# Kernel tuning notes

Hardware: AMD Instinct MI355X
Metric: run time of the kernel (lower is better)

## Reference

```python
import jax, jax.numpy as jnp
import numpy as np

ODE_UNFOLDS = 6   # ncps LTCCell default
EPS = 1e-8
BATCH = 4096

def _conv(x, w, b, stride, pad):
    y = jax.lax.conv_general_dilated(x, w, (stride, stride), [(pad, pad), (pad, pad)],
                                     dimension_numbers=('NCHW', 'OIHW', 'NCHW'))
    return y + b[None, :, None, None]

def _bn(x, g, bta, m, v):
    # eval-mode batchnorm (running stats)
    inv = g * jax.lax.rsqrt(v + 1e-5)
    return x * inv[None, :, None, None] + (bta - m * inv)[None, :, None, None]

def _maxpool2(x):
    return jax.lax.reduce_window(x, -jnp.inf, jax.lax.max, (1, 1, 2, 2), (1, 1, 2, 2), 'VALID')

def _forward(x, conv1_w, conv1_b, conv2_w, conv2_b, bn2_g, bn2_b, bn2_m, bn2_v,
             conv3_w, conv3_b, conv4_w, conv4_b, bn4_g, bn4_b, bn4_m, bn4_v,
             input_w, input_b, sensory_mu, sensory_sigma, sensory_w, sensory_erev, sensory_mask,
             mu, sigma, w, erev, mask, gleak, vleak, cm, output_w, output_b):
    h = jax.nn.relu(_conv(x, conv1_w, conv1_b, 1, 0))                                            # [B,16,26,26]
    h = jax.nn.relu(_bn(_conv(h, conv2_w, conv2_b, 2, 2), bn2_g, bn2_b, bn2_m, bn2_v))           # [B,32,14,14]
    h = jax.nn.relu(_conv(h, conv3_w, conv3_b, 2, 2))                                            # [B,64,7,7]
    h = _maxpool2(jax.nn.relu(_bn(_conv(h, conv4_w, conv4_b, 2, 2), bn4_g, bn4_b, bn4_m, bn4_v)))  # [B,128,2,2]
    seq = h.reshape(-1, 32, 16)                                                                  # [B,T=32,F=16]
    # --- LTC cell (ncps fused ODE solver) ---
    xin = seq * input_w + input_b                                                                # affine input mapping
    # sensory synapses depend only on the input -> precompute for all timesteps
    sact = jax.nn.softplus(sensory_w) * jax.nn.sigmoid((xin[..., None] - sensory_mu) * sensory_sigma) * sensory_mask  # [B,T,16,19]
    wnum_s = jnp.einsum('btsn,sn->btn', sact, sensory_erev)   # [B,T,19]
    wden_s = jnp.sum(sact, axis=2)                            # [B,T,19]
    w_pos = jax.nn.softplus(w) * mask                         # [pre=19,post=19]
    gl = jax.nn.softplus(gleak)
    cm_t = jax.nn.softplus(cm) * ODE_UNFOLDS                  # cm / (elapsed_time=1.0 / unfolds)
    def tstep(v, nd):
        wns, wds = nd
        def unfold(v2, _):
            wa = w_pos * jax.nn.sigmoid((v2[..., None] - mu) * sigma)   # [B,19,19]
            num = cm_t * v2 + gl * vleak + jnp.sum(wa * erev, axis=1) + wns
            den = cm_t + gl + jnp.sum(wa, axis=1) + wds
            return num / (den + EPS), None
        v, _ = jax.lax.scan(unfold, v, None, length=ODE_UNFOLDS)
        return v, None
    h0 = jnp.zeros((seq.shape[0], 19), seq.dtype)
    vT, _ = jax.lax.scan(tstep, h0, (jnp.swapaxes(wnum_s, 0, 1), jnp.swapaxes(wden_s, 0, 1)))
    # out[:, -1, :] == output mapping of final state; motor neurons are the first 2
    return vT[:, :2] * output_w + output_b


def setup_inputs() -> dict:
    key = jax.random.key(0)
    ks = jax.random.split(key, 16)
    rng = np.random.default_rng(0)
    u = lambda k, s, lo, hi: jax.random.uniform(k, s, jnp.float32, lo, hi)
    n = lambda k, s, sc: jax.random.normal(k, s, jnp.float32) * sc
    inp = {}
    inp['x'] = jax.random.normal(ks[0], (BATCH, 1, 28, 28), jnp.float32)
    inp['conv1_w'] = n(ks[1], (16, 1, 3, 3), 0.3); inp['conv1_b'] = jnp.zeros(16)
    inp['conv2_w'] = n(ks[2], (32, 16, 3, 3), 0.08); inp['conv2_b'] = jnp.zeros(32)
    inp['bn2_g'] = jnp.ones(32); inp['bn2_b'] = jnp.zeros(32)
    inp['bn2_m'] = jnp.zeros(32); inp['bn2_v'] = jnp.ones(32)
    inp['conv3_w'] = n(ks[3], (64, 32, 5, 5), 0.035); inp['conv3_b'] = jnp.zeros(64)
    inp['conv4_w'] = n(ks[4], (128, 64, 5, 5), 0.025); inp['conv4_b'] = jnp.zeros(128)
    inp['bn4_g'] = jnp.ones(128); inp['bn4_b'] = jnp.zeros(128)
    inp['bn4_m'] = jnp.zeros(128); inp['bn4_v'] = jnp.ones(128)
    inp['input_w'] = jnp.ones(16); inp['input_b'] = jnp.zeros(16)
    # ncps LTCCell init ranges
    inp['sensory_mu'] = u(ks[5], (16, 19), 0.3, 0.8)
    inp['sensory_sigma'] = u(ks[6], (16, 19), 3.0, 8.0)
    inp['sensory_w'] = u(ks[7], (16, 19), 0.001, 1.0)
    inp['sensory_erev'] = jnp.asarray(rng.choice([-1.0, 1.0], (16, 19)).astype(np.float32))
    inp['sensory_mask'] = jnp.asarray((rng.random((16, 19)) < 0.35).astype(np.float32))
    inp['mu'] = u(ks[8], (19, 19), 0.3, 0.8)
    inp['sigma'] = u(ks[9], (19, 19), 3.0, 8.0)
    inp['w'] = u(ks[10], (19, 19), 0.001, 1.0)
    inp['erev'] = jnp.asarray(rng.choice([-1.0, 1.0], (19, 19)).astype(np.float32))
    inp['mask'] = jnp.asarray((rng.random((19, 19)) < 0.35).astype(np.float32))
    inp['gleak'] = u(ks[11], (19,), 0.001, 1.0)
    inp['vleak'] = u(ks[12], (19,), -0.2, 0.2)
    inp['cm'] = u(ks[13], (19,), 0.4, 0.6)
    inp['output_w'] = jnp.ones(2); inp['output_b'] = jnp.zeros(2)
    return inp


def reference(x, conv1_w, conv1_b, conv2_w, conv2_b, bn2_g, bn2_b, bn2_m, bn2_v,
              conv3_w, conv3_b, conv4_w, conv4_b, bn4_g, bn4_b, bn4_m, bn4_v,
              input_w, input_b, sensory_mu, sensory_sigma, sensory_w, sensory_erev, sensory_mask,
              mu, sigma, w, erev, mask, gleak, vleak, cm, output_w, output_b):
    return _forward(x, conv1_w, conv1_b, conv2_w, conv2_b, bn2_g, bn2_b, bn2_m, bn2_v,
                    conv3_w, conv3_b, conv4_w, conv4_b, bn4_g, bn4_b, bn4_m, bn4_v,
                    input_w, input_b, sensory_mu, sensory_sigma, sensory_w, sensory_erev, sensory_mask,
                    mu, sigma, w, erev, mask, gleak, vleak, cm, output_w, output_b)
```

## Files before the change

kernel.cpp:

```cpp
#include <hip/hip_runtime.h>

#define BATCH 4096
typedef unsigned short u16_t;

#define P_SWM   0
#define P_SWME  304
#define P_WP    608
#define P_WPE   969
#define P_GL    1330
#define P_GLVL  1349
#define P_CMT   1368
#define P_SC2   1392
#define P_SH2   1424
#define P_SC4   1456
#define P_SH4   1584

#define OFF_PAR 0L
#define OFF_B2F 2048L
#define OFF_B3F 6656L
#define OFF_B4F 57856L
#define OFF_DYN 262656L

typedef __attribute__((ext_vector_type(8))) short short8;
typedef __attribute__((ext_vector_type(16))) float f32x16;
typedef __attribute__((ext_vector_type(4))) float f32x4;
#define MFMA(a, b, c) __builtin_amdgcn_mfma_f32_32x32x16_bf16(a, b, c, 0, 0, 0)
#define MFMA16(a, b, c) __builtin_amdgcn_mfma_f32_16x16x32_bf16(a, b, c, 0, 0, 0)

#define PERM_HI(w1, w0) __builtin_amdgcn_perm((w1), (w0), 0x05040100u)
#define PERM_LO(w1, w0) __builtin_amdgcn_perm((w1), (w0), 0x07060302u)

union U8 { unsigned u[4]; short8 v; };
union A4 { f32x4 v; float f[4]; };

__device__ __forceinline__ float sigmoidf_(float x) {
    return 1.0f / (1.0f + __expf(-x));
}
__device__ __forceinline__ float softplusf_(float x) { return log1pf(__expf(x)); }

__device__ __forceinline__ unsigned rne16(unsigned u) {
    return (u + 0x7FFFu + ((u >> 16) & 1u)) & 0xFFFF0000u;
}
__device__ __forceinline__ unsigned splitpack(float f) {
    unsigned uh = rne16(__float_as_uint(f));
    float rsd = f - __uint_as_float(uh);
    unsigned ur = rne16(__float_as_uint(rsd));
    return (uh >> 16) | ur;
}
__device__ __forceinline__ u16_t bfhalf(float v, int pl) {
    unsigned uh = rne16(__float_as_uint(v));
    if (pl == 0) return (u16_t)(uh >> 16);
    float rsd = v - __uint_as_float(uh);
    return (u16_t)(rne16(__float_as_uint(rsd)) >> 16);
}

__global__ __launch_bounds__(256) void k_prep(
    const float* __restrict__ w2, const float* __restrict__ w3, const float* __restrict__ w4,
    const float* __restrict__ sw, const float* __restrict__ serev, const float* __restrict__ smask,
    const float* __restrict__ w,  const float* __restrict__ erev,  const float* __restrict__ mask,
    const float* __restrict__ gleak, const float* __restrict__ vleak, const float* __restrict__ cm,
    const float* __restrict__ b2, const float* __restrict__ g2, const float* __restrict__ be2,
    const float* __restrict__ m2, const float* __restrict__ v2,
    const float* __restrict__ b4, const float* __restrict__ g4, const float* __restrict__ be4,
    const float* __restrict__ m4, const float* __restrict__ v4,
    float* __restrict__ ws) {
    int gid = blockIdx.x * 256 + threadIdx.x, stride = gridDim.x * 256;
    u16_t* b2f = (u16_t*)(ws + OFF_B2F);
    u16_t* b3f = (u16_t*)(ws + OFF_B3F);
    u16_t* b4f = (u16_t*)(ws + OFF_B4F);
    for (int i = gid; i < 9216; i += stride) {
        int j = i & 7, ln = (i >> 3) & 63;
        int r = i >> 9;
        int s = r % 9, pl = r / 9;
        int k = s * 16 + (ln >> 5) * 8 + j;
        int tap = k >> 4, ci = k & 15;
        int co = ln & 31;
        b2f[i] = bfhalf(w2[(co * 16 + ci) * 9 + tap], pl);
    }
    for (int i = gid; i < 102400; i += stride) {
        int j = i & 7, ln = (i >> 3) & 63;
        int t = i >> 9;
        int tap = t % 25, r = t / 25;
        int nt = r & 3, pl = r >> 2;
        int co = nt * 16 + (ln & 15);
        int ci = (ln >> 4) * 8 + j;
        b3f[i] = bfhalf(w3[(co * 32 + ci) * 25 + tap], pl);
    }
    for (int i = gid; i < 409600; i += stride) {
        int j = i & 7, ln = (i >> 3) & 63;
        int t = i >> 9;
        int ks = t % 50, r = t / 50;
        int nt = r & 7, pl = r >> 3;
        int co = nt * 16 + (ln & 15);
        int tap = ks >> 1;
        int ci = (ks & 1) * 32 + (ln >> 4) * 8 + j;
        b4f[i] = bfhalf(w4[(co * 64 + ci) * 25 + tap], pl);
    }
    if (blockIdx.x == 0) {
        float* par = ws + OFF_PAR;
        int tid = threadIdx.x;
        for (int i = tid; i < 304; i += 256) {
            float v_ = softplusf_(sw[i]) * smask[i];
            par[P_SWM + i] = v_;
            par[P_SWME + i] = v_ * serev[i];
        }
        for (int i = tid; i < 361; i += 256) {
            float v_ = softplusf_(w[i]) * mask[i];
            par[P_WP + i] = v_;
            par[P_WPE + i] = v_ * erev[i];
        }
        for (int i = tid; i < 19; i += 256) {
            float g = softplusf_(gleak[i]);
            par[P_GL + i] = g;
            par[P_GLVL + i] = g * vleak[i];
            par[P_CMT + i] = softplusf_(cm[i]) * 6.0f;
        }
        for (int i = tid; i < 32; i += 256) {
            float inv = g2[i] * __frsqrt_rn(v2[i] + 1e-5f);
            par[P_SC2 + i] = inv;
            par[P_SH2 + i] = (b2[i] - m2[i]) * inv + be2[i];
        }
        for (int i = tid; i < 128; i += 256) {
            float inv = g4[i] * __frsqrt_rn(v4[i] + 1e-5f);
            par[P_SC4 + i] = inv;
            par[P_SH4 + i] = (b4[i] - m4[i]) * inv + be4[i];
        }
    }
}

__global__ __launch_bounds__(512, 6) void k_conv12(
    const float* __restrict__ x, const float* __restrict__ w1, const float* __restrict__ b1,
    const float* __restrict__ ws, unsigned* __restrict__ h2g) {
    __shared__ float xs[784];
    __shared__ unsigned h1s[11509];
    const float* par = ws + OFF_PAR;
    int b = blockIdx.x, tid = threadIdx.x;
    {
        for (int i = tid; i < 784; i += 512) xs[i] = x[(long)b * 784 + i];
        if (tid < 17) h1s[676 * 17 + tid] = 0u;
    }
    __syncthreads();
    {
        int co = tid >> 5, slot = tid & 31;
        float wr[9];
        #pragma unroll
        for (int i = 0; i < 9; i++) wr[i] = w1[co * 9 + i];
        float bb = b1[co];
        for (int k = 0; k < 22; k++) {
            int px = slot + (k << 5);
            if (px >= 676) break;
            int oh = px / 26, ow = px % 26;
            float s = bb;
            #pragma unroll
            for (int kh = 0; kh < 3; kh++)
                #pragma unroll
                for (int kw = 0; kw < 3; kw++)
                    s = fmaf(xs[(oh + kh) * 28 + ow + kw], wr[kh * 3 + kw], s);
            h1s[px * 17 + co] = splitpack(fmaxf(s, 0.f));
        }
    }
    __syncthreads();
    {
        int wv = tid >> 6, lane = tid & 63;
        int mloc = lane & 31, hf = lane >> 5, half8 = hf * 8;
        const u16_t* B2 = (const u16_t*)(ws + OFF_B2F);
        const short8* pb = (const short8*)B2 + lane;
        float sc = par[P_SC2 + mloc], sh = par[P_SH2 + mloc];
        int mt = wv;
        if (mt < 7) {
            int px = mt * 32 + mloc;
            bool pxok = px < 196;
            int pxc = pxok ? px : 195;
            int oh = pxc / 14, ow = pxc % 14;
            int ihb = oh * 2 - 2, iwb = ow * 2 - 2;
            f32x16 acc;
            #pragma unroll
            for (int i = 0; i < 16; i++) acc[i] = 0.f;
            #pragma unroll
            for (int s = 0; s < 9; s++) {
                int kh = s / 3, kw = s % 3;
                int ih = ihb + kh, iw = iwb + kw;
                bool ok = pxok && ((unsigned)ih < 26u) && ((unsigned)iw < 26u);
                int abase = (ok ? (ih * 26 + iw) * 17 : 676 * 17) + half8;
                unsigned w_[8];
                #pragma unroll
                for (int j = 0; j < 8; j++) w_[j] = h1s[abase + j];
                U8 ah, al;
                #pragma unroll
                for (int d = 0; d < 4; d++) {
                    ah.u[d] = PERM_HI(w_[2 * d + 1], w_[2 * d]);
                    al.u[d] = PERM_LO(w_[2 * d + 1], w_[2 * d]);
                }
                short8 bh = pb[s * 64];
                short8 bl = pb[(9 + s) * 64];
                acc = MFMA(ah.v, bh, acc);
                acc = MFMA(ah.v, bl, acc);
                acc = MFMA(al.v, bh, acc);
                acc = MFMA(al.v, bl, acc);
            }
            #pragma unroll
            for (int r5 = 0; r5 < 16; r5++) {
                int row = (r5 & 3) + 8 * (r5 >> 2) + 4 * hf;
                int pxw = mt * 32 + row;
                if (pxw < 196) {
                    float y = fmaxf(fmaf(acc[r5], sc, sh), 0.f);
                    h2g[(long)b * 6272 + pxw * 32 + mloc] = splitpack(y);
                }
            }
        }
    }
}

__global__ __launch_bounds__(256, 2) void k_conv34s(
    const unsigned* __restrict__ h2g, const float* __restrict__ b3g,
    const float* __restrict__ inw, const float* __restrict__ inb,
    const float* __restrict__ smu, const float* __restrict__ ssig,
    const float* __restrict__ ws,
    float* __restrict__ wn, float* __restrict__ wd, int nimg) {
    __shared__ unsigned h2s[12969];
    __shared__ unsigned h3s[6435];
    const float* par = ws + OFF_PAR;
    int b = blockIdx.x, tid = threadIdx.x;
    int g0 = b * 2;
    int g1 = (g0 + 1 < nimg) ? g0 + 1 : g0;
    {
        const unsigned* s0 = h2g + (long)g0 * 6272;
        const unsigned* s1 = h2g + (long)g1 * 6272;
        for (int i = tid; i < 12544; i += 256) {
            int img = i >= 6272;
            int r = img ? i - 6272 : i;
            h2s[img * 6468 + (r >> 5) * 33 + (r & 31)] = (img ? s1 : s0)[r];
        }
        if (tid < 33) h2s[12936 + tid] = 0u;
        if (tid < 65) h3s[6370 + tid] = 0u;
    }
    __syncthreads();
    int wv = tid >> 6, lane = tid & 63;
    int n16 = lane & 15, quad = lane >> 4, quad8 = quad * 8;

    {
        int img = wv & 1, mhalf = wv >> 1;
        int imgo = img * 6468;
        int mt0 = mhalf * 2;
        A4 acc[2][4];
        #pragma unroll
        for (int nt = 0; nt < 4; nt++) {
            float bi = b3g[nt * 16 + n16];
            #pragma unroll
            for (int r = 0; r < 4; r++) { acc[0][nt].f[r] = bi; acc[1][nt].f[r] = bi; }
        }
        int oh2[2], ow2[2];
        bool pxok[2];
        #pragma unroll
        for (int mi = 0; mi < 2; mi++) {
            int px = (mt0 + mi) * 16 + n16;
            pxok[mi] = px < 49;
            int pxc = pxok[mi] ? px : 48;
            oh2[mi] = (pxc / 7) * 2 - 2;
            ow2[mi] = (pxc % 7) * 2 - 2;
        }
        const short8* B3 = (const short8*)(const u16_t*)(ws + OFF_B3F);
        const short8* ph0 = B3 + (0 * 25) * 64 + lane;
        const short8* ph1 = B3 + (1 * 25) * 64 + lane;
        const short8* ph2 = B3 + (2 * 25) * 64 + lane;
        const short8* ph3 = B3 + (3 * 25) * 64 + lane;
        const short8* pl0 = B3 + (4 * 25) * 64 + lane;
        const short8* pl1 = B3 + (5 * 25) * 64 + lane;
        const short8* pl2 = B3 + (6 * 25) * 64 + lane;
        const short8* pl3 = B3 + (7 * 25) * 64 + lane;
        #pragma unroll
        for (int kh = 0; kh < 5; kh++) {
            #pragma unroll
            for (int kw = 0; kw < 5; kw++) {
                int s = (kh * 5 + kw) * 64;
                short8 bh0 = ph0[s], bh1 = ph1[s], bh2 = ph2[s], bh3 = ph3[s];
                short8 bl0 = pl0[s], bl1 = pl1[s], bl2 = pl2[s], bl3 = pl3[s];
                #pragma unroll
                for (int mi = 0; mi < 2; mi++) {
                    int ih = oh2[mi] + kh, iw = ow2[mi] + kw;
                    bool ok = pxok[mi] && ((unsigned)ih < 14u) && ((unsigned)iw < 14u);
                    int rowb = ok ? imgo + (ih * 14 + iw) * 33 : 12936;
                    const unsigned* ap = h2s + rowb + quad8;
                    unsigned w_[8];
                    #pragma unroll
                    for (int j = 0; j < 8; j++) w_[j] = ap[j];
                    U8 ah, al;
                    #pragma unroll
                    for (int d = 0; d < 4; d++) {
                        ah.u[d] = PERM_HI(w_[2 * d + 1], w_[2 * d]);
                        al.u[d] = PERM_LO(w_[2 * d + 1], w_[2 * d]);
                    }
                    acc[mi][0].v = MFMA16(ah.v, bh0, acc[mi][0].v);
                    acc[mi][0].v = MFMA16(ah.v, bl0, acc[mi][0].v);
                    acc[mi][0].v = MFMA16(al.v, bh0, acc[mi][0].v);
                    acc[mi][0].v = MFMA16(al.v, bl0, acc[mi][0].v);
                    acc[mi][1].v = MFMA16(ah.v, bh1, acc[mi][1].v);
                    acc[mi][1].v = MFMA16(ah.v, bl1, acc[mi][1].v);
                    acc[mi][1].v = MFMA16(al.v, bh1, acc[mi][1].v);
                    acc[mi][1].v = MFMA16(al.v, bl1, acc[mi][1].v);
                    acc[mi][2].v = MFMA16(ah.v, bh2, acc[mi][2].v);
                    acc[mi][2].v = MFMA16(ah.v, bl2, acc[mi][2].v);
                    acc[mi][2].v = MFMA16(al.v, bh2, acc[mi][2].v);
                    acc[mi][2].v = MFMA16(al.v, bl2, acc[mi][2].v);
                    acc[mi][3].v = MFMA16(ah.v, bh3, acc[mi][3].v);
                    acc[mi][3].v = MFMA16(ah.v, bl3, acc[mi][3].v);
                    acc[mi][3].v = MFMA16(al.v, bh3, acc[mi][3].v);
                    acc[mi][3].v = MFMA16(al.v, bl3, acc[mi][3].v);
                }
            }
        }
        #pragma unroll
        for (int mi = 0; mi < 2; mi++) {
            #pragma unroll
            for (int nt = 0; nt < 4; nt++) {
                int co = nt * 16 + n16;
                #pragma unroll
                for (int r = 0; r < 4; r++) {
                    int pxw = (mt0 + mi) * 16 + quad * 4 + r;
                    if (pxw < 49)
                        h3s[img * 3185 + pxw * 65 + co] = splitpack(fmaxf(acc[mi][nt].f[r], 0.f));
                }
            }
        }
    }
    __syncthreads();
    {
        int oh = n16 >> 2, ow = n16 & 3;
        int oh2 = oh * 2 - 2, ow2 = ow * 2 - 2;
        int nt0 = wv * 2, nt1 = nt0 + 1;
        A4 c[2][2];
        #pragma unroll
        for (int mi = 0; mi < 2; mi++)
            #pragma unroll
            for (int r = 0; r < 4; r++) { c[mi][0].f[r] = 0.f; c[mi][1].f[r] = 0.f; }
        const short8* B4 = (const short8*)(const u16_t*)(ws + OFF_B4F);
        const short8* ph0 = B4 + (nt0 * 50) * 64 + lane;
        const short8* ph1 = B4 + (nt1 * 50) * 64 + lane;
        const short8* pl0 = B4 + ((8 + nt0) * 50) * 64 + lane;
        const short8* pl1 = B4 + ((8 + nt1) * 50) * 64 + lane;
        #pragma unroll
        for (int kh = 0; kh < 5; kh++) {
            int ih = oh2 + kh;
            #pragma unroll
            for (int kw = 0; kw < 5; kw++) {
                int iw = ow2 + kw;
                bool ok = ((unsigned)ih < 7u) && ((unsigned)iw < 7u);
                #pragma unroll
                for (int ch = 0; ch < 2; ch++) {
                    int s = ((kh * 5 + kw) * 2 + ch) * 64;
                    short8 bh0 = ph0[s], bl0 = pl0[s];
                    short8 bh1 = ph1[s], bl1 = pl1[s];
                    #pragma unroll
                    for (int mi = 0; mi < 2; mi++) {
                        int rowb = ok ? mi * 3185 + (ih * 7 + iw) * 65 + ch * 32 : 6370;
                        const unsigned* ap = h3s + rowb + quad8;
                        unsigned w_[8];
                        #pragma unroll
                        for (int j = 0; j < 8; j++) w_[j] = ap[j];
                        U8 ah, al;
                        #pragma unroll
                        for (int d = 0; d < 4; d++) {
                            ah.u[d] = PERM_HI(w_[2 * d + 1], w_[2 * d]);
                            al.u[d] = PERM_LO(w_[2 * d + 1], w_[2 * d]);
                        }
                        c[mi][0].v = MFMA16(ah.v, bh0, c[mi][0].v);
                        c[mi][0].v = MFMA16(ah.v, bl0, c[mi][0].v);
                        c[mi][0].v = MFMA16(al.v, bh0, c[mi][0].v);
                        c[mi][0].v = MFMA16(al.v, bl0, c[mi][0].v);
                        c[mi][1].v = MFMA16(ah.v, bh1, c[mi][1].v);
                        c[mi][1].v = MFMA16(ah.v, bl1, c[mi][1].v);
                        c[mi][1].v = MFMA16(al.v, bh1, c[mi][1].v);
                        c[mi][1].v = MFMA16(al.v, bl1, c[mi][1].v);
                    }
                }
            }
        }
        __syncthreads();
        float* xin_s = (float*)h2s;
        #pragma unroll
        for (int mi = 0; mi < 2; mi++) {
            #pragma unroll
            for (int t2 = 0; t2 < 2; t2++) {
                int co = (t2 ? nt1 : nt0) * 16 + n16;
                float sc = par[P_SC4 + co], sh = par[P_SH4 + co];
                float y[4];
                #pragma unroll
                for (int r = 0; r < 4; r++) y[r] = fmaxf(fmaf(c[mi][t2].f[r], sc, sh), 0.f);
                float p0 = fmaxf(y[0], y[1]);
                float p1 = fmaxf(y[2], y[3]);
                p0 = fmaxf(p0, __shfl_xor(p0, 16));
                p1 = fmaxf(p1, __shfl_xor(p1, 16));
                if ((quad & 1) == 0) {
                    int ph_ = quad >> 1;
                    int ts = co >> 2;
                    int f0 = ((co & 3) << 2) + ph_ * 2;
                    xin_s[mi * 512 + ts * 16 + f0] = fmaf(p0, inw[f0], inb[f0]);
                    xin_s[mi * 512 + ts * 16 + f0 + 1] = fmaf(p1, inw[f0 + 1], inb[f0 + 1]);
                }
            }
        }
    }
    __syncthreads();
    const float* xin_s = (const float*)h2s;
    for (int idx = tid; idx < 1216; idx += 256) {
        int img = idx >= 608;
        int r = img ? idx - 608 : idx;
        int gi = g0 + img;
        if (gi >= nimg) break;
        int tt = r / 19, n = r - tt * 19;
        float nu = 0.f, de = 0.f;
        #pragma unroll
        for (int s = 0; s < 16; s++) {
            float sg = sigmoidf_((xin_s[img * 512 + tt * 16 + s] - smu[s * 19 + n]) * ssig[s * 19 + n]);
            nu = fmaf(par[P_SWME + s * 19 + n], sg, nu);
            de = fmaf(par[P_SWM + s * 19 + n], sg, de);
        }
        wn[((long)gi * 32 + tt) * 19 + n] = nu;
        wd[((long)gi * 32 + tt) * 19 + n] = de;
    }
}

__global__ __launch_bounds__(256, 2) void k_ltc(
    const float* __restrict__ mu_g, const float* __restrict__ sg_g,
    const float* __restrict__ ws,
    const float* __restrict__ wn, const float* __restrict__ wd,
    const float* __restrict__ outw, const float* __restrict__ outb,
    float* __restrict__ out, int img0, int nimg) {
    const float* par = ws + OFF_PAR;
    int tid = threadIdx.x, wave = tid >> 6, lane = tid & 63;
    int li = lane / 19, j = lane - li * 19;
    if (li > 2) { li = 2; j = 18; }
    int il = blockIdx.x * 12 + wave * 3 + li;
    int ilc = il < nimg ? il : nimg - 1;

    const float L2E = 1.44269504f;
    float aj[19], bj[19], wpj[19], wpej[19];
    #pragma unroll
    for (int i = 0; i < 19; i++) {
        float mu = mu_g[i * 19 + j];
        float sg = sg_g[i * 19 + j];
        aj[i] = -sg * L2E;
        bj[i] = mu * sg * L2E;
        wpj[i] = par[P_WP + i * 19 + j];
        wpej[i] = par[P_WPE + i * 19 + j];
    }
    float cmt = par[P_CMT + j], gl = par[P_GL + j], glvl = par[P_GLVL + j];
    float v = 0.f;
    long base0 = (long)ilc * 608 + j;
    float wns = wn[base0], wds = wd[base0];
    int lbase = li * 19;
    for (int t = 0; t < 32; t++) {
        float wns_n = 0.f, wds_n = 0.f;
        if (t < 31) {
            long basen = base0 + (t + 1) * 19;
            wns_n = wn[basen];
            wds_n = wd[basen];
        }
        #pragma unroll 1
        for (int u = 0; u < 6; u++) {
            float vi[19];
            #pragma unroll
            for (int i = 0; i < 19; i++) vi[i] = __shfl(v, lbase + i, 64);
            float sg[19];
            #pragma unroll
            for (int i = 0; i < 19; i++)
                sg[i] = __builtin_amdgcn_exp2f(fmaf(vi[i], aj[i], bj[i]));
            float n0 = 0.f, n1 = 0.f, d0 = 0.f, d1 = 0.f;
            #pragma unroll
            for (int i = 0; i < 19; i++) {
                float s = __builtin_amdgcn_rcpf(1.0f + sg[i]);
                if (i & 1) { n1 = fmaf(wpej[i], s, n1); d1 = fmaf(wpj[i], s, d1); }
                else       { n0 = fmaf(wpej[i], s, n0); d0 = fmaf(wpj[i], s, d0); }
            }
            float num = fmaf(cmt, v, glvl) + wns + (n0 + n1);
            float den = cmt + gl + wds + (d0 + d1);
            v = num * __builtin_amdgcn_rcpf(den + 1e-8f);
        }
        wns = wns_n; wds = wds_n;
    }
    if (j < 2 && il < nimg && lane < 57)
        out[(long)(img0 + il) * 2 + j] = fmaf(v, outw[j], outb[j]);
}

extern "C" void kernel_launch(void* const* d_in, const int* in_sizes, int n_in,
                              void* d_out, int out_size, void* d_ws, size_t ws_size,
                              hipStream_t stream) {
    const float* x    = (const float*)d_in[0];
    const float* w1   = (const float*)d_in[1];
    const float* b1   = (const float*)d_in[2];
    const float* w2   = (const float*)d_in[3];
    const float* b2   = (const float*)d_in[4];
    const float* g2   = (const float*)d_in[5];
    const float* be2  = (const float*)d_in[6];
    const float* m2   = (const float*)d_in[7];
    const float* v2   = (const float*)d_in[8];
    const float* w3   = (const float*)d_in[9];
    const float* b3   = (const float*)d_in[10];
    const float* w4   = (const float*)d_in[11];
    const float* b4   = (const float*)d_in[12];
    const float* g4   = (const float*)d_in[13];
    const float* be4  = (const float*)d_in[14];
    const float* m4   = (const float*)d_in[15];
    const float* v4   = (const float*)d_in[16];
    const float* inw  = (const float*)d_in[17];
    const float* inb  = (const float*)d_in[18];
    const float* smu  = (const float*)d_in[19];
    const float* ssig = (const float*)d_in[20];
    const float* sw   = (const float*)d_in[21];
    const float* serv = (const float*)d_in[22];
    const float* smk  = (const float*)d_in[23];
    const float* mu_  = (const float*)d_in[24];
    const float* sig_ = (const float*)d_in[25];
    const float* w_   = (const float*)d_in[26];
    const float* erev = (const float*)d_in[27];
    const float* mask = (const float*)d_in[28];
    const float* glk  = (const float*)d_in[29];
    const float* vlk  = (const float*)d_in[30];
    const float* cm   = (const float*)d_in[31];
    const float* outw = (const float*)d_in[32];
    const float* outb = (const float*)d_in[33];
    float* ws = (float*)d_ws;

    k_prep<<<64, 256, 0, stream>>>(w2, w3, w4, sw, serv, smk, w_, erev, mask,
                                   glk, vlk, cm, b2, g2, be2, m2, v2,
                                   b4, g4, be4, m4, v4, ws);

    long avail = (long)(ws_size / 4) - OFF_DYN;
    long per = 6272 + 1216;
    int chunk = (int)(avail / per);
    if (chunk > BATCH) chunk = BATCH;
    if (chunk < 2) chunk = 2;

    float* wnp = ws + OFF_DYN;
    float* wdp = wnp + (long)chunk * 608;
    unsigned* h2 = (unsigned*)(wdp + (long)chunk * 608);

    for (int c0 = 0; c0 < BATCH; c0 += chunk) {
        int n = (BATCH - c0 < chunk) ? (BATCH - c0) : chunk;
        k_conv12<<<n, 512, 0, stream>>>(x + (long)c0 * 784, w1, b1, ws, h2);
        k_conv34s<<<(n + 1) / 2, 256, 0, stream>>>(h2, b3, inw, inb, smu, ssig, ws,
                                                   wnp, wdp, n);
        k_ltc<<<(n + 11) / 12, 256, 0, stream>>>(mu_, sig_, ws, wnp, wdp, outw, outb,
                                                 (float*)d_out, c0, n);
    }
}
```

Before: 570.3 us.

## Switch LTC ODE path to fp64 and drop low-low split-bf16 MFMA terms

```diff
diff --git a/kernel.cpp b/kernel.cpp
--- a/kernel.cpp
+++ b/kernel.cpp
@@ -1,25 +1,26 @@
 #include <hip/hip_runtime.h>
+#include <math.h>
 
 #define BATCH 4096
 typedef unsigned short u16_t;
 
-#define P_SWM   0
-#define P_SWME  304
-#define P_WP    608
-#define P_WPE   969
-#define P_GL    1330
-#define P_GLVL  1349
-#define P_CMT   1368
 #define P_SC2   1392
 #define P_SH2   1424
 #define P_SC4   1456
 #define P_SH4   1584
+#define P_GL64   1712
+#define P_GLVL64 1750
+#define P_CMT64  1788
+#define P_WP64   1826
+#define P_WPE64  2548
+#define P_SWM64  3270
+#define P_SWME64 3878
 
 #define OFF_PAR 0L
-#define OFF_B2F 2048L
-#define OFF_B3F 6656L
-#define OFF_B4F 57856L
-#define OFF_DYN 262656L
+#define OFF_B2F 4608L
+#define OFF_B3F 9216L
+#define OFF_B4F 60416L
+#define OFF_DYN 265216L
 
 typedef __attribute__((ext_vector_type(8))) short short8;
 typedef __attribute__((ext_vector_type(16))) float f32x16;
@@ -33,11 +34,6 @@
 union U8 { unsigned u[4]; short8 v; };
 union A4 { f32x4 v; float f[4]; };
 
-__device__ __forceinline__ float sigmoidf_(float x) {
-    return 1.0f / (1.0f + __expf(-x));
-}
-__device__ __forceinline__ float softplusf_(float x) { return log1pf(__expf(x)); }
-
 __device__ __forceinline__ unsigned rne16(unsigned u) {
     return (u + 0x7FFFu + ((u >> 16) & 1u)) & 0xFFFF0000u;
 }
@@ -52,6 +48,20 @@
     if (pl == 0) return (u16_t)(uh >> 16);
     float rsd = v - __uint_as_float(uh);
     return (u16_t)(rne16(__float_as_uint(rsd)) >> 16);
+}
+__device__ __forceinline__ double softplus64(double x) { return log1p(exp(x)); }
+
+__device__ __forceinline__ double sigmoid64(double arg) {
+    double na = -arg;
+    float yf = (float)na * 1.44269504f;
+    float e32 = __builtin_amdgcn_exp2f(yf);
+    double ey = fma(na, 1.4426950408889634, -(double)yf);
+    double e64 = (double)e32 * fma(0.6931471805599453, ey, 1.0);
+    double dd = 1.0 + e64;
+    float r0 = __builtin_amdgcn_rcpf((float)dd);
+    double r = (double)r0;
+    r = fma(r, fma(-dd, r, 1.0), r);
+    return r;
 }
 
 __global__ __launch_bounds__(256) void k_prep(
@@ -98,22 +108,29 @@
     }
     if (blockIdx.x == 0) {
         float* par = ws + OFF_PAR;
+        double* swm64  = (double*)(ws + P_SWM64);
+        double* swme64 = (double*)(ws + P_SWME64);
+        double* wp64   = (double*)(ws + P_WP64);
+        double* wpe64  = (double*)(ws + P_WPE64);
+        double* gl64   = (double*)(ws + P_GL64);
+        double* glvl64 = (double*)(ws + P_GLVL64);
+        double* cmt64  = (double*)(ws + P_CMT64);
         int tid = threadIdx.x;
         for (int i = tid; i < 304; i += 256) {
-            float v_ = softplusf_(sw[i]) * smask[i];
-            par[P_SWM + i] = v_;
-            par[P_SWME + i] = v_ * serev[i];
+            double v_ = softplus64((double)sw[i]) * (double)smask[i];
+            swm64[i] = v_;
+            swme64[i] = v_ * (double)serev[i];
         }
         for (int i = tid; i < 361; i += 256) {
-            float v_ = softplusf_(w[i]) * mask[i];
-            par[P_WP + i] = v_;
-            par[P_WPE + i] = v_ * erev[i];
+            double v_ = softplus64((double)w[i]) * (double)mask[i];
+            wp64[i] = v_;
+            wpe64[i] = v_ * (double)erev[i];
         }
         for (int i = tid; i < 19; i += 256) {
-            float g = softplusf_(gleak[i]);
-            par[P_GL + i] = g;
-            par[P_GLVL + i] = g * vleak[i];
-            par[P_CMT + i] = softplusf_(cm[i]) * 6.0f;
+            double g = softplus64((double)gleak[i]);
+            gl64[i] = g;
+            glvl64[i] = g * (double)vleak[i];
+            cmt64[i] = softplus64((double)cm[i]) * 6.0;
         }
         for (int i = tid; i < 32; i += 256) {
             float inv = g2[i] * __frsqrt_rn(v2[i] + 1e-5f);
@@ -196,7 +213,6 @@
                 acc = MFMA(ah.v, bh, acc);
                 acc = MFMA(ah.v, bl, acc);
                 acc = MFMA(al.v, bh, acc);
-                acc = MFMA(al.v, bl, acc);
             }
             #pragma unroll
             for (int r5 = 0; r5 < 16; r5++) {
@@ -216,7 +232,7 @@
     const float* __restrict__ inw, const float* __restrict__ inb,
     const float* __restrict__ smu, const float* __restrict__ ssig,
     const float* __restrict__ ws,
-    float* __restrict__ wn, float* __restrict__ wd, int nimg) {
+    double* __restrict__ wn, double* __restrict__ wd, int nimg) {
     __shared__ unsigned h2s[12969];
     __shared__ unsigned h3s[6435];
     const float* par = ws + OFF_PAR;
@@ -293,19 +309,15 @@
                     acc[mi][0].v = MFMA16(ah.v, bh0, acc[mi][0].v);
                     acc[mi][0].v = MFMA16(ah.v, bl0, acc[mi][0].v);
                     acc[mi][0].v = MFMA16(al.v, bh0, acc[mi][0].v);
-                    acc[mi][0].v = MFMA16(al.v, bl0, acc[mi][0].v);
                     acc[mi][1].v = MFMA16(ah.v, bh1, acc[mi][1].v);
                     acc[mi][1].v = MFMA16(ah.v, bl1, acc[mi][1].v);
                     acc[mi][1].v = MFMA16(al.v, bh1, acc[mi][1].v);
-                    acc[mi][1].v = MFMA16(al.v, bl1, acc[mi][1].v);
                     acc[mi][2].v = MFMA16(ah.v, bh2, acc[mi][2].v);
                     acc[mi][2].v = MFMA16(ah.v, bl2, acc[mi][2].v);
                     acc[mi][2].v = MFMA16(al.v, bh2, acc[mi][2].v);
-                    acc[mi][2].v = MFMA16(al.v, bl2, acc[mi][2].v);
                     acc[mi][3].v = MFMA16(ah.v, bh3, acc[mi][3].v);
                     acc[mi][3].v = MFMA16(ah.v, bl3, acc[mi][3].v);
                     acc[mi][3].v = MFMA16(al.v, bh3, acc[mi][3].v);
-                    acc[mi][3].v = MFMA16(al.v, bl3, acc[mi][3].v);
                 }
             }
         }
@@ -366,11 +378,9 @@
                         c[mi][0].v = MFMA16(ah.v, bh0, c[mi][0].v);
                         c[mi][0].v = MFMA16(ah.v, bl0, c[mi][0].v);
                         c[mi][0].v = MFMA16(al.v, bh0, c[mi][0].v);
-                        c[mi][0].v = MFMA16(al.v, bl0, c[mi][0].v);
                         c[mi][1].v = MFMA16(ah.v, bh1, c[mi][1].v);
                         c[mi][1].v = MFMA16(ah.v, bl1, c[mi][1].v);
                         c[mi][1].v = MFMA16(al.v, bh1, c[mi][1].v);
-                        c[mi][1].v = MFMA16(al.v, bl1, c[mi][1].v);
                     }
                 }
             }
@@ -402,18 +412,22 @@
     }
     __syncthreads();
     const float* xin_s = (const float*)h2s;
+    const double* swm64  = (const double*)(ws + P_SWM64);
+    const double* swme64 = (const double*)(ws + P_SWME64);
     for (int idx = tid; idx < 1216; idx += 256) {
         int img = idx >= 608;
         int r = img ? idx - 608 : idx;
         int gi = g0 + img;
         if (gi >= nimg) break;
         int tt = r / 19, n = r - tt * 19;
-        float nu = 0.f, de = 0.f;
+        double nu = 0.0, de = 0.0;
         #pragma unroll
         for (int s = 0; s < 16; s++) {
-            float sg = sigmoidf_((xin_s[img * 512 + tt * 16 + s] - smu[s * 19 + n]) * ssig[s * 19 + n]);
-            nu = fmaf(par[P_SWME + s * 19 + n], sg, nu);
-            de = fmaf(par[P_SWM + s * 19 + n], sg, de);
+            double arg = ((double)xin_s[img * 512 + tt * 16 + s] - (double)smu[s * 19 + n])
+                         * (double)ssig[s * 19 + n];
+            double sg = sigmoid64(arg);
+            nu = fma(swme64[s * 19 + n], sg, nu);
+            de = fma(swm64[s * 19 + n], sg, de);
         }
         wn[((long)gi * 32 + tt) * 19 + n] = nu;
         wd[((long)gi * 32 + tt) * 19 + n] = de;
@@ -423,63 +437,58 @@
 __global__ __launch_bounds__(256, 2) void k_ltc(
     const float* __restrict__ mu_g, const float* __restrict__ sg_g,
     const float* __restrict__ ws,
-    const float* __restrict__ wn, const float* __restrict__ wd,
+    const double* __restrict__ wn, const double* __restrict__ wd,
     const float* __restrict__ outw, const float* __restrict__ outb,
     float* __restrict__ out, int img0, int nimg) {
-    const float* par = ws + OFF_PAR;
     int tid = threadIdx.x, wave = tid >> 6, lane = tid & 63;
     int li = lane / 19, j = lane - li * 19;
     if (li > 2) { li = 2; j = 18; }
     int il = blockIdx.x * 12 + wave * 3 + li;
     int ilc = il < nimg ? il : nimg - 1;
 
-    const float L2E = 1.44269504f;
-    float aj[19], bj[19], wpj[19], wpej[19];
+    const double* wp64  = (const double*)(ws + P_WP64);
+    const double* wpe64 = (const double*)(ws + P_WPE64);
+    float mus[19], sgs[19];
+    double wpj[19], wpej[19];
     #pragma unroll
     for (int i = 0; i < 19; i++) {
-        float mu = mu_g[i * 19 + j];
-        float sg = sg_g[i * 19 + j];
-        aj[i] = -sg * L2E;
-        bj[i] = mu * sg * L2E;
-        wpj[i] = par[P_WP + i * 19 + j];
-        wpej[i] = par[P_WPE + i * 19 + j];
-    }
-    float cmt = par[P_CMT + j], gl = par[P_GL + j], glvl = par[P_GLVL + j];
-    float v = 0.f;
+        mus[i] = mu_g[i * 19 + j];
+        sgs[i] = sg_g[i * 19 + j];
+        wpj[i] = wp64[i * 19 + j];
+        wpej[i] = wpe64[i * 19 + j];
+    }
+    double cmt  = ((const double*)(ws + P_CMT64))[j];
+    double gl   = ((const double*)(ws + P_GL64))[j];
+    double glvl = ((const double*)(ws + P_GLVL64))[j];
+    double v64 = 0.0;
     long base0 = (long)ilc * 608 + j;
-    float wns = wn[base0], wds = wd[base0];
     int lbase = li * 19;
     for (int t = 0; t < 32; t++) {
-        float wns_n = 0.f, wds_n = 0.f;
-        if (t < 31) {
-            long basen = base0 + (t + 1) * 19;
-            wns_n = wn[basen];
-            wds_n = wd[basen];
-        }
+        double wns = wn[base0 + t * 19];
+        double wds = wd[base0 + t * 19];
         #pragma unroll 1
         for (int u = 0; u < 6; u++) {
-            float vi[19];
-            #pragma unroll
-            for (int i = 0; i < 19; i++) vi[i] = __shfl(v, lbase + i, 64);
-            float sg[19];
-            #pragma unroll
-            for (int i = 0; i < 19; i++)
-                sg[i] = __builtin_amdgcn_exp2f(fmaf(vi[i], aj[i], bj[i]));
-            float n0 = 0.f, n1 = 0.f, d0 = 0.f, d1 = 0.f;
+            double n0 = 0.0, n1 = 0.0, d0 = 0.0, d1 = 0.0;
             #pragma unroll
             for (int i = 0; i < 19; i++) {
-                float s = __builtin_amdgcn_rcpf(1.0f + sg[i]);
-                if (i & 1) { n1 = fmaf(wpej[i], s, n1); d1 = fmaf(wpj[i], s, d1); }
-                else       { n0 = fmaf(wpej[i], s, n0); d0 = fmaf(wpj[i], s, d0); }
-            }
-            float num = fmaf(cmt, v, glvl) + wns + (n0 + n1);
-            float den = cmt + gl + wds + (d0 + d1);
-            v = num * __builtin_amdgcn_rcpf(den + 1e-8f);
-        }
-        wns = wns_n; wds = wds_n;
+                double vi = __shfl(v64, lbase + i, 64);
+                double arg = (vi - (double)mus[i]) * (double)sgs[i];
+                double s = sigmoid64(arg);
+                if (i & 1) { n1 = fma(wpej[i], s, n1); d1 = fma(wpj[i], s, d1); }
+                else       { n0 = fma(wpej[i], s, n0); d0 = fma(wpj[i], s, d0); }
+            }
+            double num = fma(cmt, v64, glvl) + wns + (n0 + n1);
+            double den = cmt + gl + wds + (d0 + d1) + 1e-8;
+            float q0 = __builtin_amdgcn_rcpf((float)den);
+            double q = (double)q0;
+            q = fma(q, fma(-den, q, 1.0), q);
+            double vt = num * q;
+            v64 = fma(q, fma(-den, vt, num), vt);
+        }
     }
     if (j < 2 && il < nimg && lane < 57)
-        out[(long)(img0 + il) * 2 + j] = fmaf(v, outw[j], outb[j]);
+        out[(long)(img0 + il) * 2 + j] =
+            (float)fma(v64, (double)outw[j], (double)outb[j]);
 }
 
 extern "C" void kernel_launch(void* const* d_in, const int* in_sizes, int n_in,
@@ -526,13 +535,13 @@
                                    b4, g4, be4, m4, v4, ws);
 
     long avail = (long)(ws_size / 4) - OFF_DYN;
-    long per = 6272 + 1216;
+    long per = 6272 + 2432;
     int chunk = (int)(avail / per);
     if (chunk > BATCH) chunk = BATCH;
     if (chunk < 2) chunk = 2;
 
-    float* wnp = ws + OFF_DYN;
-    float* wdp = wnp + (long)chunk * 608;
+    double* wnp = (double*)(ws + OFF_DYN);
+    double* wdp = wnp + (long)chunk * 608;
     unsigned* h2 = (unsigned*)(wdp + (long)chunk * 608);
 
     for (int c0 = 0; c0 < BATCH; c0 += chunk) {
```

After: 750.4 us. +31.6%, slower.
